# Kernel tuning notes

Measured on AMD Instinct MI355X. Metric: run time of the kernel, lower is better.

## Reference

```python
import jax, jax.numpy as jnp
import numpy as np

N, K, D, E, H, O = 8192, 16, 256, 128, 512, 256


def _mlp(v, W1, W2):
    # nn.Sequential(Linear(no bias), Tanh, Linear(no bias)) with torch [out,in] weights
    return jnp.tanh(v @ W1.T) @ W2.T


def setup_inputs() -> dict:
    key = jax.random.key(0)
    ks = jax.random.split(key, 16)
    def rn(k, shape, s=1.0):
        return jax.random.normal(k, shape, jnp.float32) * s
    return {
        "x": rn(ks[0], (N, D)),
        "neibs": rn(ks[1], (N * K, D)),
        "edge_emb": rn(ks[2], (N * K, E)),
        "mask": jax.random.randint(ks[3], (N, K), 0, 2, jnp.int32),
        "W1x": rn(ks[4], (H, D), 0.02), "W2x": rn(ks[5], (H, H), 0.02),
        "W1n": rn(ks[6], (H, D), 0.02), "W2n": rn(ks[7], (H, H), 0.02),
        "W1e": rn(ks[8], (H, E), 0.02), "W2e": rn(ks[9], (H, H), 0.02),
        "Wfx": rn(ks[10], (O, D), 0.02), "bfx": jnp.zeros((O,), jnp.float32),
        "Wfn": rn(ks[11], (O, D), 0.02), "bfn": jnp.zeros((O,), jnp.float32),
        "Wfe": rn(ks[12], (O, E), 0.02), "bfe": jnp.zeros((O,), jnp.float32),
    }


def reference(x, neibs, edge_emb, mask, W1x, W2x, W1n, W2n, W1e, W2e,
              Wfx, bfx, Wfn, bfn, Wfe, bfe):
    n, d = x.shape
    e = edge_emb.shape[1]
    x_att = _mlp(x, W1x, W2x)                                  # [N,H]
    neib_att = _mlp(neibs, W1n, W2n).reshape(n, -1, H)         # [N,K,H]
    edge_att = _mlp(edge_emb, W1e, W2e).reshape(n, -1, H)      # [N,K,H]

    # node-neighbor attention (scaled by hard-coded sqrt(512))
    ws = jnp.einsum('nkh,nh->nk', neib_att, x_att) / np.sqrt(512.0).astype(np.float32)
    ws = jax.nn.softmax(ws, axis=1)
    agg_neib = jnp.einsum('nk,nkd->nd', ws, neibs.reshape(n, -1, d))
    out = jnp.concatenate([x @ Wfx.T + bfx, agg_neib @ Wfn.T + bfn], axis=1)

    # node-edge attention (unscaled, masked)
    ws2 = jnp.einsum('nkh,nh->nk', edge_att, x_att)
    ws2 = ws2 + (-9999999.0) * mask.astype(x.dtype)
    ws2 = jax.nn.softmax(ws2, axis=1)
    agg_edge = jnp.einsum('nk,nke->ne', ws2, edge_emb.reshape(n, -1, e))
    out = jnp.concatenate([out, agg_edge @ Wfe.T + bfe], axis=1)  # [N,3*O]
    return jax.nn.relu(out)
```

## Files before the change

kernel.cpp:

```cpp
#include <hip/hip_runtime.h>
#include <hip/hip_bf16.h>

typedef __bf16 bf16;
typedef __bf16 bf16x2 __attribute__((ext_vector_type(2)));
typedef __bf16 bf16x4 __attribute__((ext_vector_type(4)));
typedef __bf16 bf16x8 __attribute__((ext_vector_type(8)));
typedef float  f32x4  __attribute__((ext_vector_type(4)));

__device__ __forceinline__ void async16(const bf16* g, bf16* l) {
  __builtin_amdgcn_global_load_lds(
      (__attribute__((address_space(1))) void*)g,
      (__attribute__((address_space(3))) void*)l,
      16, 0, 0);
}

__device__ __forceinline__ void fence_barrier() {
  asm volatile("s_waitcnt vmcnt(0) lgkmcnt(0)" ::: "memory");
  __syncthreads();
}

__device__ __forceinline__ float fast_tanh(float x) {
  float e = __builtin_amdgcn_exp2f(x * 2.88539008177793f);
  return 1.f - 2.f * __builtin_amdgcn_rcpf(e + 1.f);
}

__device__ __forceinline__ int swz(int elem, int row) {
  return elem ^ ((row & 7) << 3);
}

template<int ACT, typename OT>
__global__ __launch_bounds__(256, 4)
void gemm64(const bf16* __restrict__ A, const bf16* __restrict__ W,
            OT* __restrict__ C, int K, int ldc, float alpha,
            const float* __restrict__ bias) {
  __shared__ bf16 As[64 * 64];
  __shared__ bf16 Bs[64 * 64];
  const int tid  = threadIdx.x;
  const int wave = tid >> 6, lane = tid & 63;
  const int wr = wave >> 1, wc = wave & 1;
  const int g = lane >> 4, l4 = lane & 15;

  f32x4 acc[2][2];
#pragma unroll
  for (int i = 0; i < 2; ++i)
#pragma unroll
    for (int j = 0; j < 2; ++j)
      acc[i][j] = (f32x4){0.f, 0.f, 0.f, 0.f};

  const bf16* Abase = A + (size_t)blockIdx.x * 64 * K;
  const bf16* Wbase = W + (size_t)blockIdx.y * 64 * K;

  for (int k0 = 0; k0 < K; k0 += 64) {
#pragma unroll
    for (int i = 0; i < 2; ++i) {
      const int cb  = i * 256 + wave * 64;
      const int c   = cb + lane;
      const int row = c >> 3;
      const int kk  = ((c & 7) ^ (row & 7)) << 3;
      async16(Abase + (size_t)row * K + k0 + kk, &As[cb * 8]);
      async16(Wbase + (size_t)row * K + k0 + kk, &Bs[cb * 8]);
    }
    fence_barrier();
#pragma unroll
    for (int s = 0; s < 2; ++s) {
      const int koff = s * 32 + g * 8;
      bf16x8 af[2], bfr[2];
#pragma unroll
      for (int i = 0; i < 2; ++i) {
        const int ra = wr * 32 + i * 16 + l4;
        af[i] = *(const bf16x8*)&As[ra * 64 + swz(koff, ra)];
      }
#pragma unroll
      for (int j = 0; j < 2; ++j) {
        const int rb = wc * 32 + j * 16 + l4;
        bfr[j] = *(const bf16x8*)&Bs[rb * 64 + swz(koff, rb)];
      }
#pragma unroll
      for (int i = 0; i < 2; ++i)
#pragma unroll
        for (int j = 0; j < 2; ++j)
          acc[i][j] = __builtin_amdgcn_mfma_f32_16x16x32_bf16(af[i], bfr[j], acc[i][j], 0, 0, 0);
    }
    fence_barrier();
  }

  const int rbase = blockIdx.x * 64 + wr * 32;
  const int cbase = blockIdx.y * 64 + wc * 32;
#pragma unroll
  for (int i = 0; i < 2; ++i)
#pragma unroll
    for (int j = 0; j < 2; ++j) {
      const int col = cbase + j * 16 + l4;
      const float bv = bias ? bias[col] : 0.f;
#pragma unroll
      for (int r = 0; r < 4; ++r) {
        const int row = rbase + i * 16 + g * 4 + r;
        float v = acc[i][j][r] * alpha + bv;
        if (ACT == 1) v = fast_tanh(v);
        if (ACT == 2) v = fmaxf(v, 0.f);
        C[(size_t)row * ldc + col] = (OT)v;
      }
    }
}

template<int D>
__global__ __launch_bounds__(256, 2)
void score_agg(const float* __restrict__ A, const bf16* __restrict__ Wb,
               const bf16* __restrict__ y, int ldy, int yoff, float scale,
               const int* __restrict__ mask, bf16* __restrict__ agg) {
  __shared__ bf16 As[64 * D];
  __shared__ bf16 Bs[256 * 64];
  float* sred = (float*)Bs;
  float* wgt  = (float*)Bs + 256;
  const int tid  = threadIdx.x;
  const int wave = tid >> 6, lane = tid & 63;
  const int g = lane >> 4, l4 = lane & 15;
  const int blk = blockIdx.x;

  const float* Ab = A + (size_t)blk * 64 * D;
  constexpr int F4PR = D / 4;
#pragma unroll
  for (int ii = 0; ii < D / 16; ++ii) {
    const int c    = ii * 256 + tid;
    const int row  = c / F4PR;
    const int col4 = (c % F4PR) * 4;
    const float4 v = *(const float4*)(Ab + (size_t)row * D + col4);
    bf16x4 o = {(bf16)v.x, (bf16)v.y, (bf16)v.z, (bf16)v.w};
    *(bf16x4*)&As[row * D + swz(col4, row)] = o;
  }

  float p[4][4];
#pragma unroll
  for (int i = 0; i < 4; ++i)
#pragma unroll
    for (int r = 0; r < 4; ++r) p[i][r] = 0.f;

  fence_barrier();

  for (int j = 0; j < 2; ++j) {
    const bf16* Wj = Wb + (size_t)j * 256 * D;
    f32x4 acc[4][4];
#pragma unroll
    for (int i = 0; i < 4; ++i)
#pragma unroll
      for (int jj = 0; jj < 4; ++jj)
        acc[i][jj] = (f32x4){0.f, 0.f, 0.f, 0.f};

    for (int k0 = 0; k0 < D; k0 += 64) {
#pragma unroll
      for (int i = 0; i < 8; ++i) {
        const int cb  = i * 256 + wave * 64;
        const int c   = cb + lane;
        const int row = c >> 3;
        const int kk  = ((c & 7) ^ (row & 7)) << 3;
        async16(Wj + (size_t)row * D + k0 + kk, &Bs[cb * 8]);
      }
      fence_barrier();
#pragma unroll
      for (int s = 0; s < 2; ++s) {
        const int koff = s * 32 + g * 8;
        bf16x8 af[4], bfr[4];
#pragma unroll
        for (int i = 0; i < 4; ++i) {
          const int ra = i * 16 + l4;
          af[i] = *(const bf16x8*)&As[ra * D + swz(k0 + koff, ra)];
        }
#pragma unroll
        for (int jj = 0; jj < 4; ++jj) {
          const int rb = wave * 64 + jj * 16 + l4;
          bfr[jj] = *(const bf16x8*)&Bs[rb * 64 + swz(koff, rb)];
        }
#pragma unroll
        for (int i = 0; i < 4; ++i)
#pragma unroll
          for (int jj = 0; jj < 4; ++jj)
            acc[i][jj] = __builtin_amdgcn_mfma_f32_16x16x32_bf16(af[i], bfr[jj], acc[i][jj], 0, 0, 0);
      }
      fence_barrier();
    }

#pragma unroll
    for (int i = 0; i < 4; ++i) {
      const size_t yb = (size_t)(blk * 4 + i) * ldy + yoff + j * 256 + wave * 64;
#pragma unroll
      for (int jj = 0; jj < 4; ++jj) {
        const float yv = (float)y[yb + jj * 16 + l4];
        p[i][0] += fast_tanh(acc[i][jj][0]) * yv;
        p[i][1] += fast_tanh(acc[i][jj][1]) * yv;
        p[i][2] += fast_tanh(acc[i][jj][2]) * yv;
        p[i][3] += fast_tanh(acc[i][jj][3]) * yv;
      }
    }
  }

#pragma unroll
  for (int i = 0; i < 4; ++i)
#pragma unroll
    for (int r = 0; r < 4; ++r) {
      float v = p[i][r];
#pragma unroll
      for (int m = 1; m < 16; m <<= 1) v += __shfl_xor(v, m);
      p[i][r] = v;
    }
  if (l4 == 0) {
#pragma unroll
    for (int i = 0; i < 4; ++i)
#pragma unroll
      for (int r = 0; r < 4; ++r)
        sred[wave * 64 + i * 16 + g * 4 + r] = p[i][r];
  }
  __syncthreads();

  if (tid < 64) {
    const int node_g = blk * 4 + (tid >> 4);
    float s = (sred[tid] + sred[64 + tid] + sred[128 + tid] + sred[192 + tid]) * scale;
    if (mask) s -= 9999999.0f * (float)mask[node_g * 16 + (tid & 15)];
    float m = s;
#pragma unroll
    for (int d = 1; d < 16; d <<= 1) m = fmaxf(m, __shfl_xor(m, d));
    float e = __builtin_amdgcn_exp2f((s - m) * 1.44269504088896f);
    float sum = e;
#pragma unroll
    for (int d = 1; d < 16; d <<= 1) sum += __shfl_xor(sum, d);
    wgt[tid] = e / sum;
  }
  __syncthreads();

  constexpr int EPT = D / 64;
  const int n  = tid >> 6;
  const int dl = (tid & 63) * EPT;
  float a[EPT];
#pragma unroll
  for (int e = 0; e < EPT; ++e) a[e] = 0.f;
#pragma unroll
  for (int k = 0; k < 16; ++k) {
    const float w = wgt[n * 16 + k];
    const int rk = n * 16 + k;
    if constexpr (EPT == 4) {
      bf16x4 v = *(const bf16x4*)&As[rk * D + swz(dl, rk)];
      a[0] += w * (float)v[0]; a[1] += w * (float)v[1];
      a[2] += w * (float)v[2]; a[3] += w * (float)v[3];
    } else {
      bf16x2 v = *(const bf16x2*)&As[rk * D + swz(dl, rk)];
      a[0] += w * (float)v[0]; a[1] += w * (float)v[1];
    }
  }
  if constexpr (EPT == 4) {
    bf16x4 o = {(bf16)a[0], (bf16)a[1], (bf16)a[2], (bf16)a[3]};
    *(bf16x4*)&agg[(size_t)(blk * 4 + n) * D + dl] = o;
  } else {
    bf16x2 o = {(bf16)a[0], (bf16)a[1]};
    *(bf16x2*)&agg[(size_t)(blk * 4 + n) * D + dl] = o;
  }
}

struct CvtEnt { const float* s; bf16* d; int n; };
struct CvtArgs { CvtEnt e[8]; };

__global__ void cvt_small(CvtArgs args) {
  const CvtEnt ent = args.e[blockIdx.y];
  const int i = blockIdx.x * 2048 + threadIdx.x * 8;
  if (i < ent.n) {
    const float4 a = *(const float4*)(ent.s + i);
    const float4 c = *(const float4*)(ent.s + i + 4);
    bf16x8 o = { (bf16)a.x, (bf16)a.y, (bf16)a.z, (bf16)a.w,
                 (bf16)c.x, (bf16)c.y, (bf16)c.z, (bf16)c.w };
    *(bf16x8*)(ent.d + i) = o;
  }
}

__global__ void transpose2(const float* __restrict__ s0, bf16* __restrict__ d0,
                           const float* __restrict__ s1, bf16* __restrict__ d1) {
  __shared__ float t[16][17];
  const float* s = blockIdx.z ? s1 : s0;
  bf16* d = blockIdx.z ? d1 : d0;
  const int x0 = blockIdx.x * 16, y0 = blockIdx.y * 16;
  t[threadIdx.y][threadIdx.x] = s[(size_t)(y0 + threadIdx.y) * 512 + x0 + threadIdx.x];
  __syncthreads();
  d[(size_t)(x0 + threadIdx.y) * 512 + (y0 + threadIdx.x)] = (bf16)t[threadIdx.x][threadIdx.y];
}

extern "C" void kernel_launch(void* const* d_in, const int* in_sizes, int n_in,
                              void* d_out, int out_size, void* d_ws, size_t ws_size,
                              hipStream_t stream) {
  const float* x     = (const float*)d_in[0];
  const float* neibs = (const float*)d_in[1];
  const float* edge  = (const float*)d_in[2];
  const int*   mask  = (const int*)d_in[3];
  const float* W1x = (const float*)d_in[4];
  const float* W2x = (const float*)d_in[5];
  const float* W1n = (const float*)d_in[6];
  const float* W2n = (const float*)d_in[7];
  const float* W1e = (const float*)d_in[8];
  const float* W2e = (const float*)d_in[9];
  const float* Wfx = (const float*)d_in[10];
  const float* bfx = (const float*)d_in[11];
  const float* Wfn = (const float*)d_in[12];
  const float* bfn = (const float*)d_in[13];
  const float* Wfe = (const float*)d_in[14];
  const float* bfe = (const float*)d_in[15];
  float* out = (float*)d_out;

  char* wsb = (char*)d_ws;
  const size_t MB = 1024 * 1024;
  bf16* W2nT = (bf16*)(wsb + 0);
  bf16* W2eT = (bf16*)(wsb + 512 * 1024);
  char* wtb  = wsb + 1 * MB;
  bf16* W1xb = (bf16*)(wtb + 0);
  bf16* W2xb = (bf16*)(wtb + 256 * 1024);
  bf16* W1nb = (bf16*)(wtb + 768 * 1024);
  bf16* W1eb = (bf16*)(wtb + 1024 * 1024);
  bf16* Wfxb = (bf16*)(wtb + 1152 * 1024);
  bf16* Wfnb = (bf16*)(wtb + 1280 * 1024);
  bf16* Wfeb = (bf16*)(wtb + 1408 * 1024);
  bf16* xb    = (bf16*)(wsb + 3 * MB);
  bf16* h_x   = (bf16*)(wsb + 7 * MB);
  bf16* x_att = (bf16*)(wsb + 15 * MB);
  bf16* ycat  = (bf16*)(wsb + 23 * MB);
  bf16* aggn  = (bf16*)(wsb + 39 * MB);
  bf16* agge  = (bf16*)(wsb + 43 * MB);

  const float inv_sqrt512 = 0.04419417382415922f;

  CvtArgs ca;
  ca.e[0] = {x,   xb,   2097152};
  ca.e[1] = {W1x, W1xb, 131072};
  ca.e[2] = {W2x, W2xb, 262144};
  ca.e[3] = {W1n, W1nb, 131072};
  ca.e[4] = {W1e, W1eb, 65536};
  ca.e[5] = {Wfx, Wfxb, 65536};
  ca.e[6] = {Wfn, Wfnb, 65536};
  ca.e[7] = {Wfe, Wfeb, 32768};
  cvt_small<<<dim3(1024, 8), 256, 0, stream>>>(ca);

  transpose2<<<dim3(32, 32, 2), dim3(16, 16), 0, stream>>>(W2n, W2nT, W2e, W2eT);

  gemm64<1, bf16><<<dim3(128, 8), 256, 0, stream>>>(xb, W1xb, h_x, 256, 512, 1.f, nullptr);
  gemm64<0, bf16><<<dim3(128, 8), 256, 0, stream>>>(h_x, W2xb, x_att, 512, 512, 1.f, nullptr);
  gemm64<0, bf16><<<dim3(128, 16), 256, 0, stream>>>(x_att, W2nT, ycat, 512, 1024, 1.f, nullptr);

  score_agg<256><<<2048, 256, 0, stream>>>(neibs, W1nb, ycat, 1024, 0, inv_sqrt512, nullptr, aggn);
  score_agg<128><<<2048, 256, 0, stream>>>(edge,  W1eb, ycat, 1024, 512, 1.f, mask, agge);

  gemm64<2, float><<<dim3(128, 4), 256, 0, stream>>>(xb,   Wfxb, out + 0,   256, 768, 1.f, bfx);
  gemm64<2, float><<<dim3(128, 4), 256, 0, stream>>>(aggn, Wfnb, out + 256, 256, 768, 1.f, bfn);
  gemm64<2, float><<<dim3(128, 4), 256, 0, stream>>>(agge, Wfeb, out + 512, 128, 768, 1.f, bfe);
}
```

Before: 395.3 us.

## Double-buffer weight tiles in gemm64 and score_agg to overlap loads with MFMA

```diff
diff --git a/kernel.cpp b/kernel.cpp
--- a/kernel.cpp
+++ b/kernel.cpp
@@ -14,6 +14,17 @@
       16, 0, 0);
 }
 
+template<int N>
+__device__ __forceinline__ void vm_wait() {
+  asm volatile("s_waitcnt vmcnt(%0)" :: "i"(N) : "memory");
+}
+
+__device__ __forceinline__ void hard_barrier() {
+  asm volatile("" ::: "memory");
+  __builtin_amdgcn_s_barrier();
+  asm volatile("" ::: "memory");
+}
+
 __device__ __forceinline__ void fence_barrier() {
   asm volatile("s_waitcnt vmcnt(0) lgkmcnt(0)" ::: "memory");
   __syncthreads();
@@ -33,8 +44,8 @@
 void gemm64(const bf16* __restrict__ A, const bf16* __restrict__ W,
             OT* __restrict__ C, int K, int ldc, float alpha,
             const float* __restrict__ bias) {
-  __shared__ bf16 As[64 * 64];
-  __shared__ bf16 Bs[64 * 64];
+  __shared__ bf16 As[2][64 * 64];
+  __shared__ bf16 Bs[2][64 * 64];
   const int tid  = threadIdx.x;
   const int wave = tid >> 6, lane = tid & 63;
   const int wr = wave >> 1, wc = wave & 1;
@@ -50,17 +61,25 @@
   const bf16* Abase = A + (size_t)blockIdx.x * 64 * K;
   const bf16* Wbase = W + (size_t)blockIdx.y * 64 * K;
 
-  for (int k0 = 0; k0 < K; k0 += 64) {
+  auto stage = [&](int buf, int k0) {
 #pragma unroll
     for (int i = 0; i < 2; ++i) {
       const int cb  = i * 256 + wave * 64;
       const int c   = cb + lane;
       const int row = c >> 3;
       const int kk  = ((c & 7) ^ (row & 7)) << 3;
-      async16(Abase + (size_t)row * K + k0 + kk, &As[cb * 8]);
-      async16(Wbase + (size_t)row * K + k0 + kk, &Bs[cb * 8]);
-    }
-    fence_barrier();
+      async16(Abase + (size_t)row * K + k0 + kk, &As[buf][cb * 8]);
+      async16(Wbase + (size_t)row * K + k0 + kk, &Bs[buf][cb * 8]);
+    }
+  };
+
+  const int nt = K >> 6;
+  stage(0, 0);
+  for (int t = 0; t < nt; ++t) {
+    const int buf = t & 1;
+    if (t + 1 < nt) { stage(buf ^ 1, (t + 1) * 64); vm_wait<4>(); }
+    else            { vm_wait<0>(); }
+    hard_barrier();
 #pragma unroll
     for (int s = 0; s < 2; ++s) {
       const int koff = s * 32 + g * 8;
@@ -68,12 +87,12 @@
 #pragma unroll
       for (int i = 0; i < 2; ++i) {
         const int ra = wr * 32 + i * 16 + l4;
-        af[i] = *(const bf16x8*)&As[ra * 64 + swz(koff, ra)];
+        af[i] = *(const bf16x8*)&As[buf][ra * 64 + swz(koff, ra)];
       }
 #pragma unroll
       for (int j = 0; j < 2; ++j) {
         const int rb = wc * 32 + j * 16 + l4;
-        bfr[j] = *(const bf16x8*)&Bs[rb * 64 + swz(koff, rb)];
+        bfr[j] = *(const bf16x8*)&Bs[buf][rb * 64 + swz(koff, rb)];
       }
 #pragma unroll
       for (int i = 0; i < 2; ++i)
@@ -81,7 +100,7 @@
         for (int j = 0; j < 2; ++j)
           acc[i][j] = __builtin_amdgcn_mfma_f32_16x16x32_bf16(af[i], bfr[j], acc[i][j], 0, 0, 0);
     }
-    fence_barrier();
+    hard_barrier();
   }
 
   const int rbase = blockIdx.x * 64 + wr * 32;
@@ -109,13 +128,31 @@
                const bf16* __restrict__ y, int ldy, int yoff, float scale,
                const int* __restrict__ mask, bf16* __restrict__ agg) {
   __shared__ bf16 As[64 * D];
-  __shared__ bf16 Bs[256 * 64];
-  float* sred = (float*)Bs;
-  float* wgt  = (float*)Bs + 256;
+  __shared__ bf16 Bs[2][256 * 32];
+  float* sred = (float*)(&Bs[0][0]);
+  float* wgt  = (float*)(&Bs[0][0]) + 256;
   const int tid  = threadIdx.x;
   const int wave = tid >> 6, lane = tid & 63;
   const int g = lane >> 4, l4 = lane & 15;
   const int blk = blockIdx.x;
+
+  constexpr int NP = D / 32;
+  constexpr int NS = 2 * NP;
+
+  auto stageB = [&](int s, int buf) {
+    const int j  = s / NP, ph = s % NP;
+    const bf16* Wsrc = Wb + (size_t)j * 256 * D + ph * 32;
+#pragma unroll
+    for (int i = 0; i < 4; ++i) {
+      const int cb  = i * 256 + wave * 64;
+      const int c   = cb + lane;
+      const int row = c >> 2;
+      const int sl  = (c & 3) ^ ((row >> 1) & 3);
+      async16(Wsrc + (size_t)row * D + sl * 8, &Bs[buf][cb * 8]);
+    }
+  };
+
+  stageB(0, 0);
 
   const float* Ab = A + (size_t)blk * 64 * D;
   constexpr int F4PR = D / 4;
@@ -137,8 +174,8 @@
 
   fence_barrier();
 
+  int s = 0;
   for (int j = 0; j < 2; ++j) {
-    const bf16* Wj = Wb + (size_t)j * 256 * D;
     f32x4 acc[4][4];
 #pragma unroll
     for (int i = 0; i < 4; ++i)
@@ -146,37 +183,34 @@
       for (int jj = 0; jj < 4; ++jj)
         acc[i][jj] = (f32x4){0.f, 0.f, 0.f, 0.f};
 
-    for (int k0 = 0; k0 < D; k0 += 64) {
-#pragma unroll
-      for (int i = 0; i < 8; ++i) {
-        const int cb  = i * 256 + wave * 64;
-        const int c   = cb + lane;
-        const int row = c >> 3;
-        const int kk  = ((c & 7) ^ (row & 7)) << 3;
-        async16(Wj + (size_t)row * D + k0 + kk, &Bs[cb * 8]);
-      }
-      fence_barrier();
-#pragma unroll
-      for (int s = 0; s < 2; ++s) {
-        const int koff = s * 32 + g * 8;
-        bf16x8 af[4], bfr[4];
-#pragma unroll
-        for (int i = 0; i < 4; ++i) {
-          const int ra = i * 16 + l4;
-          af[i] = *(const bf16x8*)&As[ra * D + swz(k0 + koff, ra)];
-        }
-#pragma unroll
-        for (int jj = 0; jj < 4; ++jj) {
-          const int rb = wave * 64 + jj * 16 + l4;
-          bfr[jj] = *(const bf16x8*)&Bs[rb * 64 + swz(koff, rb)];
-        }
-#pragma unroll
-        for (int i = 0; i < 4; ++i)
-#pragma unroll
-          for (int jj = 0; jj < 4; ++jj)
-            acc[i][jj] = __builtin_amdgcn_mfma_f32_16x16x32_bf16(af[i], bfr[jj], acc[i][jj], 0, 0, 0);
-      }
-      fence_barrier();
+#pragma unroll
+    for (int ph = 0; ph < NP; ++ph) {
+      const int buf = s & 1;
+      if (s + 1 < NS) { stageB(s + 1, buf ^ 1); vm_wait<4>(); }
+      else            { vm_wait<0>(); }
+      hard_barrier();
+
+      const int ka = ph * 32 + g * 8;
+      bf16x8 af[4], bfr[4];
+#pragma unroll
+      for (int i = 0; i < 4; ++i) {
+        const int ra = i * 16 + l4;
+        af[i] = *(const bf16x8*)&As[ra * D + swz(ka, ra)];
+      }
+#pragma unroll
+      for (int jj = 0; jj < 4; ++jj) {
+        const int rb = wave * 64 + jj * 16 + l4;
+        const int sl = g ^ ((rb >> 1) & 3);
+        bfr[jj] = *(const bf16x8*)&Bs[buf][rb * 32 + sl * 8];
+      }
+#pragma unroll
+      for (int i = 0; i < 4; ++i)
+#pragma unroll
+        for (int jj = 0; jj < 4; ++jj)
+          acc[i][jj] = __builtin_amdgcn_mfma_f32_16x16x32_bf16(af[i], bfr[jj], acc[i][jj], 0, 0, 0);
+
+      hard_barrier();
+      ++s;
     }
 
 #pragma unroll
@@ -213,12 +247,12 @@
 
   if (tid < 64) {
     const int node_g = blk * 4 + (tid >> 4);
-    float s = (sred[tid] + sred[64 + tid] + sred[128 + tid] + sred[192 + tid]) * scale;
-    if (mask) s -= 9999999.0f * (float)mask[node_g * 16 + (tid & 15)];
-    float m = s;
+    float sv = (sred[tid] + sred[64 + tid] + sred[128 + tid] + sred[192 + tid]) * scale;
+    if (mask) sv -= 9999999.0f * (float)mask[node_g * 16 + (tid & 15)];
+    float m = sv;
 #pragma unroll
     for (int d = 1; d < 16; d <<= 1) m = fmaxf(m, __shfl_xor(m, d));
-    float e = __builtin_amdgcn_exp2f((s - m) * 1.44269504088896f);
+    float e = __builtin_amdgcn_exp2f((sv - m) * 1.44269504088896f);
     float sum = e;
 #pragma unroll
     for (int d = 1; d < 16; d <<= 1) sum += __shfl_xor(sum, d);
```

Result: no change. 395.5 us (+0.0%).
